# Optimization experiments

Measured on AMD Instinct MI355X. Metric: run time of the kernel, lower is better.

Reference implementation:

```python
import jax, jax.numpy as jnp
import numpy as np

EPS = 1e-5

def _layernorm(x, g, b):
    m = jnp.mean(x, axis=-1, keepdims=True)
    v = jnp.mean((x - m) ** 2, axis=-1, keepdims=True)
    return (x - m) * jax.lax.rsqrt(v + EPS) * g + b

def setup_inputs() -> dict:
    key = jax.random.key(0)
    ks = jax.random.split(key, 6)
    B, N, D, H, F = 4, 4096, 256, 256, 1024
    s = lambda d: 1.0 / np.sqrt(d)
    return {
        "x": jax.random.normal(ks[0], (B, N, D), jnp.float32),
        "ln1_g": jnp.ones((D,), jnp.float32),
        "ln1_b": jnp.zeros((D,), jnp.float32),
        "wq": jax.random.normal(ks[1], (D, H), jnp.float32) * s(D),
        "bq": jnp.zeros((H,), jnp.float32),
        "wk": jax.random.normal(ks[2], (D, H), jnp.float32) * s(D),
        "bk": jnp.zeros((H,), jnp.float32),
        "wv": jax.random.normal(ks[3], (D, D), jnp.float32) * s(D),
        "bv": jnp.zeros((D,), jnp.float32),
        "ln2_g": jnp.ones((D,), jnp.float32),
        "ln2_b": jnp.zeros((D,), jnp.float32),
        "w1": jax.random.normal(ks[4], (D, F), jnp.float32) * s(D),
        "b1": jnp.zeros((F,), jnp.float32),
        "w2": jax.random.normal(ks[5], (F, D), jnp.float32) * s(F),
        "b2": jnp.zeros((D,), jnp.float32),
    }

def reference(x, ln1_g, ln1_b, wq, bq, wk, bk, wv, bv, ln2_g, ln2_b, w1, b1, w2, b2):
    hdim = wq.shape[1]
    x = _layernorm(x, ln1_g, ln1_b)                      # [B,N,D]
    q = x @ wq + bq                                      # [B,N,H]
    k = x @ wk + bk                                      # [B,N,H]
    v = x @ wv + bv                                      # [B,N,D]
    att = jnp.einsum('bnh,bmh->bnm', q, k) / jnp.sqrt(jnp.float32(hdim))
    att = jax.nn.softmax(att, axis=-1)                   # [B,N,N]
    x = jnp.einsum('bnm,bmd->bnd', att, v) + x           # residual around attention
    h = _layernorm(x, ln2_g, ln2_b)
    h = jax.nn.relu(h @ w1 + b1) @ w2 + b2
    return h + x
```

## Files before the change

### kernel.cpp

```cpp
#include <hip/hip_runtime.h>
#include <stdint.h>

typedef unsigned short u16;
typedef __attribute__((ext_vector_type(8))) short short8;
typedef __attribute__((ext_vector_type(4))) float f32x4;
typedef __attribute__((ext_vector_type(16))) float f32x16;

__device__ __forceinline__ u16 f2b(float f){
  union { float f; unsigned u; } x; x.f = f;
  unsigned r = x.u + 0x7FFFu + ((x.u >> 16) & 1u);
  return (u16)(r >> 16);
}

__device__ __forceinline__ unsigned cvtpk_bf16(float lo, float hi){
  unsigned r;
  asm("v_cvt_pk_bf16_f32 %0, %1, %2" : "=v"(r) : "v"(lo), "v"(hi));
  return r;
}

__device__ __forceinline__ void gload_lds16(const void* g, void* l){
  __builtin_amdgcn_global_load_lds(
      (const __attribute__((address_space(1))) unsigned int*)g,
      (__attribute__((address_space(3))) unsigned int*)l, 16, 0, 0);
}

__global__ void __launch_bounds__(256) transpose_all(const float* __restrict__ wq,
                                                     const float* __restrict__ wk,
                                                     const float* __restrict__ wv,
                                                     const float* __restrict__ w1,
                                                     const float* __restrict__ w2,
                                                     u16* __restrict__ wqkvT,
                                                     u16* __restrict__ w1T,
                                                     u16* __restrict__ w2T){
  __shared__ float sm[32][33];
  int id = blockIdx.x;
  const float* in; u16* out; int K, N, kx, ny;
  if (id < 192){
    int j = id >> 6, r = id & 63;
    in = (j==0) ? wq : (j==1) ? wk : wv;
    out = wqkvT + (size_t)j*65536; K = 256; N = 256; kx = r>>3; ny = r&7;
  } else if (id < 448){
    int r = id - 192; in = w1; out = w1T; K = 256; N = 1024; kx = r&7; ny = r>>3;
  } else {
    int r = id - 448; in = w2; out = w2T; K = 1024; N = 256; kx = r>>3; ny = r&7;
  }
  int k0 = kx*32, n0 = ny*32;
  int t = threadIdx.x; int tr = t>>5, tc = t&31;
  #pragma unroll
  for (int p=0;p<4;p++) sm[p*8+tr][tc] = in[(size_t)(k0+p*8+tr)*N + n0+tc];
  __syncthreads();
  #pragma unroll
  for (int p=0;p<4;p++) out[(size_t)(n0+p*8+tr)*K + k0+tc] = f2b(sm[tc][p*8+tr]);
}

__global__ void __launch_bounds__(256) ln_kernel(const float* __restrict__ in,
                                                 const float* __restrict__ g,
                                                 const float* __restrict__ bb,
                                                 float* __restrict__ outF,
                                                 u16* __restrict__ outB){
  int row = blockIdx.x, t = threadIdx.x;
  size_t base = (size_t)row*256;
  float v = in[base + t];
  float s = v;
  #pragma unroll
  for (int m=1;m<64;m<<=1) s += __shfl_xor(s, m);
  __shared__ float red[4];
  int w = t>>6;
  if ((t&63)==0) red[w] = s;
  __syncthreads();
  float mean = (red[0]+red[1]+red[2]+red[3]) * (1.0f/256.0f);
  float d = v - mean;
  float s2 = d*d;
  #pragma unroll
  for (int m=1;m<64;m<<=1) s2 += __shfl_xor(s2, m);
  __syncthreads();
  if ((t&63)==0) red[w] = s2;
  __syncthreads();
  float var = (red[0]+red[1]+red[2]+red[3]) * (1.0f/256.0f);
  float y = d * rsqrtf(var + 1e-5f) * g[t] + bb[t];
  if (outF) outF[base+t] = y;
  outB[base+t] = f2b(y);
}

template<int MODE>
__global__ void __launch_bounds__(256, 2) gemm_bt(const u16* __restrict__ A,
                                                  const u16* __restrict__ BT,
                                                  const float* __restrict__ bias,
                                                  const float* __restrict__ bias2,
                                                  const float* __restrict__ bias3,
                                                  const float* __restrict__ res,
                                                  float* __restrict__ outF,
                                                  u16* __restrict__ outB,
                                                  u16* __restrict__ outB2,
                                                  u16* __restrict__ outB3,
                                                  int M, int N, int K){
  __shared__ u16 As[128*64];
  __shared__ u16 Bs[128*64];
  int tid = threadIdx.x;
  int m0 = blockIdx.x*128, n0 = blockIdx.y*128;
  int wave = tid>>6, lane = tid&63, lr = lane&15, lg = lane>>4;
  int wm = (wave>>1)*64, wn = (wave&1)*64;

  f32x4 acc[4][4];
  #pragma unroll
  for (int i=0;i<4;i++)
    #pragma unroll
    for (int j=0;j<4;j++) acc[i][j] = (f32x4){0.f,0.f,0.f,0.f};

  int nk = K >> 6;
  for (int kt=0; kt<nk; ++kt){
    __syncthreads();
    #pragma unroll
    for (int i=0;i<4;i++){
      int de = i*256 + tid; int row = de>>3; int ch = de&7; int sc = ch ^ (row&7);
      gload_lds16(A + (size_t)(m0+row)*K + kt*64 + sc*8, (char*)As + de*16);
    }
    #pragma unroll
    for (int i=0;i<4;i++){
      int de = i*256 + tid; int row = de>>3; int ch = de&7; int sc = ch ^ (row&7);
      gload_lds16(BT + (size_t)(n0+row)*K + kt*64 + sc*8, (char*)Bs + de*16);
    }
    asm volatile("s_waitcnt vmcnt(0)" ::: "memory");
    __syncthreads();
    #pragma unroll
    for (int kk=0;kk<2;kk++){
      short8 af[4], bf[4];
      #pragma unroll
      for (int mi=0;mi<4;mi++){
        int row = wm + mi*16 + lr;
        int c = (kk*4 + lg) ^ (row&7);
        af[mi] = *(const short8*)&As[row*64 + c*8];
      }
      #pragma unroll
      for (int ni=0;ni<4;ni++){
        int row = wn + ni*16 + lr;
        int c = (kk*4 + lg) ^ (row&7);
        bf[ni] = *(const short8*)&Bs[row*64 + c*8];
      }
      #pragma unroll
      for (int mi=0;mi<4;mi++)
        #pragma unroll
        for (int ni=0;ni<4;ni++)
          acc[mi][ni] = __builtin_amdgcn_mfma_f32_16x16x32_bf16(af[mi], bf[ni], acc[mi][ni], 0,0,0);
    }
  }
  #pragma unroll
  for (int mi=0;mi<4;mi++)
    #pragma unroll
    for (int ni=0;ni<4;ni++)
      #pragma unroll
      for (int r=0;r<4;r++){
        int row = m0 + wm + mi*16 + lg*4 + r;
        int col = n0 + wn + ni*16 + lr;
        if (MODE==3){
          int seg = n0 >> 8;
          int c2 = col & 255;
          float bb = (seg==0) ? bias[c2] : (seg==1) ? bias2[c2] : bias3[c2];
          float vout = acc[mi][ni][r] + bb;
          if (seg==0)      outB [(size_t)row*256 + c2] = f2b(vout);
          else if (seg==1) outB2[(size_t)row*256 + c2] = f2b(vout);
          else {
            size_t gaddr = ((size_t)(row>>12)<<20)
                         + ((((size_t)((row&4095)>>3)<<8) + (size_t)c2)<<3) + (row&7);
            outB3[gaddr] = f2b(vout);
          }
        } else {
          float vout = acc[mi][ni][r] + bias[col];
          if (MODE==1) vout = fmaxf(vout, 0.f);
          if (MODE==2) outF[(size_t)row*N + col] = vout + res[(size_t)row*N + col];
          else         outB[(size_t)row*N + col] = f2b(vout);
        }
      }
}

__device__ __forceinline__ void stage_tiles(const u16* __restrict__ Kb,
                                            const u16* __restrict__ Vt,
                                            int b, int kv0,
                                            char* Kdst, char* Vdst, int tid){
  #pragma unroll
  for (int i=0;i<4;i++){
    int de = i*256 + tid; int kv = de>>5; int c = de&31; int sc = c ^ (kv&7);
    gload_lds16(Kb + (((size_t)(b*4096 + kv0 + kv))<<8) + sc*8, Kdst + (size_t)de*16);
  }
  #pragma unroll
  for (int i=0;i<4;i++){
    int de = i*256 + tid; int kvc = de>>8; int d = de&255;
    gload_lds16(Vt + ((((size_t)b*512 + (kv0>>3) + kvc)<<8) + (size_t)d)*8,
                Vdst + (size_t)de*16);
  }
}

__global__ void __launch_bounds__(256, 2) flash_attn32(const u16* __restrict__ Qb,
                                                       const u16* __restrict__ Kb,
                                                       const u16* __restrict__ Vt,
                                                       u16* __restrict__ Opart,
                                                       float* __restrict__ MLpart){
  __shared__ __align__(16) char smem[74752];
  const int NC = 4096;
  int tid = threadIdx.x, wave = tid>>6, lane = tid&63;
  int lq = lane & 31, hi = lane >> 5;
  int b = blockIdx.y, s = blockIdx.z;
  int qb0 = blockIdx.x*128 + wave*32;
  int kvbeg = s*1024;
  const int NT = 32;
  u16* PsW = (u16*)(smem + 65536) + wave*32*36;

  short8 qf[16];
  {
    const u16* qbase = Qb + (((size_t)b*NC + qb0 + lq)<<8) + hi*8;
    #pragma unroll
    for (int ks=0; ks<16; ks++) qf[ks] = *(const short8*)(qbase + ks*16);
  }

  f32x16 o[8];
  #pragma unroll
  for (int i=0;i<8;i++)
    o[i] = (f32x16){0.f,0.f,0.f,0.f,0.f,0.f,0.f,0.f,0.f,0.f,0.f,0.f,0.f,0.f,0.f,0.f};
  float mrun = -__builtin_inff(), ell = 0.f;

  stage_tiles(Kb, Vt, b, kvbeg, smem, smem + 16384, tid);
  asm volatile("s_waitcnt vmcnt(0)" ::: "memory");
  __syncthreads();

  for (int t=0; t<NT; t++){
    char* Kc = smem + ((t&1) ? 32768 : 0);
    char* Vc = Kc + 16384;
    char* Kn = smem + ((t&1) ? 0 : 32768);
    char* Vn = Kn + 16384;
    int kv0 = kvbeg + t*32;
    if (t+1 < NT) stage_tiles(Kb, Vt, b, kv0+32, Kn, Vn, tid);

    f32x16 sacc = (f32x16){0.f,0.f,0.f,0.f,0.f,0.f,0.f,0.f,0.f,0.f,0.f,0.f,0.f,0.f,0.f,0.f};
    __builtin_amdgcn_s_setprio(1);
    #pragma unroll
    for (int ks=0; ks<16; ks++){
      int c = ks*2 + hi;
      short8 kf = *(const short8*)(Kc + lq*512 + ((c ^ (lq&7))<<4));
      sacc = __builtin_amdgcn_mfma_f32_32x32x16_bf16(kf, qf[ks], sacc, 0,0,0);
    }
    __builtin_amdgcn_s_setprio(0);

    float tmax = sacc[0];
    #pragma unroll
    for (int r=1;r<16;r++) tmax = fmaxf(tmax, sacc[r]);
    tmax *= 0.0625f;
    tmax = fmaxf(tmax, __shfl_xor(tmax, 32));
    if (!__all(tmax <= mrun + 8.f)){
      float mn = fmaxf(mrun, tmax);
      float sc = __expf(mrun - mn);
      mrun = mn; ell *= sc;
      #pragma unroll
      for (int r=0;r<16;r++){
        float scr = __shfl(sc, (r&3)+8*(r>>2)+4*hi);
        #pragma unroll
        for (int dt=0; dt<8; dt++) o[dt][r] *= scr;
      }
    }

    float rs = 0.f;
    #pragma unroll
    for (int h=0; h<2; h++){
      float p[8];
      #pragma unroll
      for (int r=0;r<8;r++){ p[r] = __expf(sacc[h*8+r]*0.0625f - mrun); rs += p[r]; }
      uint2 w0, w1;
      w0.x = cvtpk_bf16(p[0], p[1]);  w0.y = cvtpk_bf16(p[2], p[3]);
      w1.x = cvtpk_bf16(p[4], p[5]);  w1.y = cvtpk_bf16(p[6], p[7]);
      *(uint2*)(PsW + lq*36 + h*16 + hi*4)     = w0;
      *(uint2*)(PsW + lq*36 + h*16 + 8 + hi*4) = w1;
    }
    rs += __shfl_xor(rs, 32);
    ell += rs;
    asm volatile("s_waitcnt lgkmcnt(0)" ::: "memory");
    __builtin_amdgcn_sched_barrier(0);
    union { uint2 u2[2]; short8 s8; } pc0, pc1;
    pc0.u2[0] = *(const uint2*)(PsW + lq*36 + hi*8);
    pc0.u2[1] = *(const uint2*)(PsW + lq*36 + hi*8 + 4);
    pc1.u2[0] = *(const uint2*)(PsW + lq*36 + 16 + hi*8);
    pc1.u2[1] = *(const uint2*)(PsW + lq*36 + 16 + hi*8 + 4);
    short8 pa0 = pc0.s8, pa1 = pc1.s8;

    __builtin_amdgcn_s_setprio(1);
    #pragma unroll
    for (int dt=0; dt<8; dt++){
      short8 vf0 = *(const short8*)(Vc + (((hi  )*256 + dt*32 + lq)<<4));
      short8 vf1 = *(const short8*)(Vc + (((2+hi)*256 + dt*32 + lq)<<4));
      o[dt] = __builtin_amdgcn_mfma_f32_32x32x16_bf16(pa0, vf0, o[dt], 0,0,0);
      o[dt] = __builtin_amdgcn_mfma_f32_32x32x16_bf16(pa1, vf1, o[dt], 0,0,0);
    }
    __builtin_amdgcn_s_setprio(0);

    asm volatile("s_waitcnt vmcnt(0)" ::: "memory");
    __syncthreads();
  }

  size_t rowb = (size_t)s*16384 + (size_t)b*NC + qb0;
  #pragma unroll
  for (int dt=0; dt<8; dt++)
    #pragma unroll
    for (int r=0;r<16;r++){
      int q = (r&3) + 8*(r>>2) + 4*hi;
      Opart[(rowb + q)*256 + dt*32 + lq] = f2b(o[dt][r]);
    }
  if (lane < 32){
    MLpart[(rowb + lane)*2]     = mrun;
    MLpart[(rowb + lane)*2 + 1] = ell;
  }
}

__global__ void __launch_bounds__(256) merge4_ln(const u16* __restrict__ Opart,
                                                 const float* __restrict__ MLpart,
                                                 const float* __restrict__ xln,
                                                 const float* __restrict__ g2,
                                                 const float* __restrict__ be2,
                                                 float* __restrict__ x2,
                                                 u16* __restrict__ h2){
  int row = blockIdx.x; int t = threadIdx.x;
  const size_t RS = 16384ull*256;
  float m[4], l[4];
  #pragma unroll
  for (int s=0;s<4;s++){
    m[s] = MLpart[((size_t)s*16384 + row)*2];
    l[s] = MLpart[((size_t)s*16384 + row)*2 + 1];
  }
  float M = fmaxf(fmaxf(m[0],m[1]), fmaxf(m[2],m[3]));
  float e[4]; float den = 0.f;
  #pragma unroll
  for (int s=0;s<4;s++){ e[s] = __expf(m[s]-M); den += l[s]*e[s]; }
  float inv = 1.0f/den;
  size_t idx = (size_t)row*256 + t;
  float v = 0.f;
  #pragma unroll
  for (int s=0;s<4;s++){
    unsigned u = Opart[(size_t)s*RS + idx];
    v += __uint_as_float(u << 16) * e[s];
  }
  v = v*inv + xln[idx];
  x2[idx] = v;
  float s1 = v;
  #pragma unroll
  for (int mk=1;mk<64;mk<<=1) s1 += __shfl_xor(s1, mk);
  __shared__ float red[4];
  int w = t>>6;
  if ((t&63)==0) red[w] = s1;
  __syncthreads();
  float mean = (red[0]+red[1]+red[2]+red[3]) * (1.0f/256.0f);
  float d = v - mean;
  float s2 = d*d;
  #pragma unroll
  for (int mk=1;mk<64;mk<<=1) s2 += __shfl_xor(s2, mk);
  __syncthreads();
  if ((t&63)==0) red[w] = s2;
  __syncthreads();
  float var = (red[0]+red[1]+red[2]+red[3]) * (1.0f/256.0f);
  h2[idx] = f2b(d * rsqrtf(var + 1e-5f) * g2[t] + be2[t]);
}

extern "C" void kernel_launch(void* const* d_in, const int* in_sizes, int n_in,
                              void* d_out, int out_size, void* d_ws, size_t ws_size,
                              hipStream_t stream){
  const float* x   = (const float*)d_in[0];
  const float* g1  = (const float*)d_in[1];
  const float* be1 = (const float*)d_in[2];
  const float* wq  = (const float*)d_in[3];
  const float* bq  = (const float*)d_in[4];
  const float* wk  = (const float*)d_in[5];
  const float* bk  = (const float*)d_in[6];
  const float* wv  = (const float*)d_in[7];
  const float* bv  = (const float*)d_in[8];
  const float* g2  = (const float*)d_in[9];
  const float* be2 = (const float*)d_in[10];
  const float* w1  = (const float*)d_in[11];
  const float* bm1 = (const float*)d_in[12];
  const float* w2  = (const float*)d_in[13];
  const float* bm2 = (const float*)d_in[14];
  float* out = (float*)d_out;

  const size_t RS = 16384ull*256;
  char* p = (char*)d_ws;
  float* xln = (float*)p;  p += RS*4;
  u16*  Op   = (u16*)p;    p += 4*RS*2;
  float* ML  = (float*)p;  p += 4*16384ull*2*4;
  u16* xb  = (u16*)p; p += RS*2;
  u16* qb  = (u16*)p; p += RS*2;
  u16* kb  = (u16*)p; p += RS*2;
  u16* vT  = (u16*)p; p += RS*2;
  u16* wqkvT = (u16*)p; p += 3*65536ull*2;
  u16* w1T = (u16*)p; p += 262144ull*2;
  u16* w2T = (u16*)p; p += 262144ull*2;
  float* x2 = xln;
  u16*   h1 = Op;
  u16*   h2 = qb;

  transpose_all<<<704, 256, 0, stream>>>(wq, wk, wv, w1, w2, wqkvT, w1T, w2T);

  ln_kernel<<<16384,256,0,stream>>>(x, g1, be1, xln, xb);

  gemm_bt<3><<<dim3(128,6),256,0,stream>>>(xb, wqkvT, bq, bk, bv, nullptr, nullptr,
                                           qb, kb, vT, 16384,768,256);

  flash_attn32<<<dim3(32,4,4),256,0,stream>>>(qb, kb, vT, Op, ML);
  merge4_ln<<<16384,256,0,stream>>>(Op, ML, xln, g2, be2, x2, h2);

  gemm_bt<1><<<dim3(128,8),256,0,stream>>>(h2, w1T, bm1, nullptr, nullptr, nullptr, nullptr,
                                           h1, nullptr, nullptr, 16384,1024,256);
  gemm_bt<2><<<dim3(128,2),256,0,stream>>>(h1, w2T, bm2, nullptr, nullptr, x2, out,
                                           nullptr, nullptr, nullptr, 16384,256,1024);
}
```

Before: 168.7 us.

## Recompute LN1 in merge, store residual as bf16, use exp2 softmax

The fp32 LN1 output is no longer written to workspace. The merge kernel recomputes LN1 from x, and the post-attention residual x2 is stored as bf16 instead of fp32 for the final GEMM epilogue. This cuts HBM write and read traffic across several kernels. The softmax switches to exp2 with a folded log2e scale constant and a rescale threshold adjusted to match. Storing the residual in bf16 adds rounding error to the final output.

```diff
diff --git a/kernel.cpp b/kernel.cpp
--- a/kernel.cpp
+++ b/kernel.cpp
@@ -10,6 +10,9 @@
   union { float f; unsigned u; } x; x.f = f;
   unsigned r = x.u + 0x7FFFu + ((x.u >> 16) & 1u);
   return (u16)(r >> 16);
+}
+__device__ __forceinline__ float b2f(u16 u){
+  return __uint_as_float(((unsigned)u) << 16);
 }
 
 __device__ __forceinline__ unsigned cvtpk_bf16(float lo, float hi){
@@ -56,7 +59,6 @@
 __global__ void __launch_bounds__(256) ln_kernel(const float* __restrict__ in,
                                                  const float* __restrict__ g,
                                                  const float* __restrict__ bb,
-                                                 float* __restrict__ outF,
                                                  u16* __restrict__ outB){
   int row = blockIdx.x, t = threadIdx.x;
   size_t base = (size_t)row*256;
@@ -77,9 +79,7 @@
   if ((t&63)==0) red[w] = s2;
   __syncthreads();
   float var = (red[0]+red[1]+red[2]+red[3]) * (1.0f/256.0f);
-  float y = d * rsqrtf(var + 1e-5f) * g[t] + bb[t];
-  if (outF) outF[base+t] = y;
-  outB[base+t] = f2b(y);
+  outB[base+t] = f2b(d * rsqrtf(var + 1e-5f) * g[t] + bb[t]);
 }
 
 template<int MODE>
@@ -88,7 +88,7 @@
                                                   const float* __restrict__ bias,
                                                   const float* __restrict__ bias2,
                                                   const float* __restrict__ bias3,
-                                                  const float* __restrict__ res,
+                                                  const u16* __restrict__ res,
                                                   float* __restrict__ outF,
                                                   u16* __restrict__ outB,
                                                   u16* __restrict__ outB2,
@@ -167,7 +167,7 @@
         } else {
           float vout = acc[mi][ni][r] + bias[col];
           if (MODE==1) vout = fmaxf(vout, 0.f);
-          if (MODE==2) outF[(size_t)row*N + col] = vout + res[(size_t)row*N + col];
+          if (MODE==2) outF[(size_t)row*N + col] = vout + b2f(res[(size_t)row*N + col]);
           else         outB[(size_t)row*N + col] = f2b(vout);
         }
       }
@@ -197,6 +197,7 @@
                                                        float* __restrict__ MLpart){
   __shared__ __align__(16) char smem[74752];
   const int NC = 4096;
+  const float C2 = 0.09016844005555897f;
   int tid = threadIdx.x, wave = tid>>6, lane = tid&63;
   int lq = lane & 31, hi = lane >> 5;
   int b = blockIdx.y, s = blockIdx.z;
@@ -243,11 +244,11 @@
     float tmax = sacc[0];
     #pragma unroll
     for (int r=1;r<16;r++) tmax = fmaxf(tmax, sacc[r]);
-    tmax *= 0.0625f;
+    tmax *= C2;
     tmax = fmaxf(tmax, __shfl_xor(tmax, 32));
-    if (!__all(tmax <= mrun + 8.f)){
+    if (!__all(tmax <= mrun + 11.5f)){
       float mn = fmaxf(mrun, tmax);
-      float sc = __expf(mrun - mn);
+      float sc = exp2f(mrun - mn);
       mrun = mn; ell *= sc;
       #pragma unroll
       for (int r=0;r<16;r++){
@@ -262,7 +263,7 @@
     for (int h=0; h<2; h++){
       float p[8];
       #pragma unroll
-      for (int r=0;r<8;r++){ p[r] = __expf(sacc[h*8+r]*0.0625f - mrun); rs += p[r]; }
+      for (int r=0;r<8;r++){ p[r] = exp2f(fmaf(sacc[h*8+r], C2, -mrun)); rs += p[r]; }
       uint2 w0, w1;
       w0.x = cvtpk_bf16(p[0], p[1]);  w0.y = cvtpk_bf16(p[2], p[3]);
       w1.x = cvtpk_bf16(p[4], p[5]);  w1.y = cvtpk_bf16(p[6], p[7]);
@@ -310,13 +311,36 @@
 
 __global__ void __launch_bounds__(256) merge4_ln(const u16* __restrict__ Opart,
                                                  const float* __restrict__ MLpart,
-                                                 const float* __restrict__ xln,
+                                                 const float* __restrict__ x,
+                                                 const float* __restrict__ g1,
+                                                 const float* __restrict__ be1,
                                                  const float* __restrict__ g2,
                                                  const float* __restrict__ be2,
-                                                 float* __restrict__ x2,
+                                                 u16* __restrict__ x2b,
                                                  u16* __restrict__ h2){
   int row = blockIdx.x; int t = threadIdx.x;
   const size_t RS = 16384ull*256;
+  size_t idx = (size_t)row*256 + t;
+  __shared__ float red[4];
+  int w = t>>6;
+
+  float xv = x[idx];
+  float s1 = xv;
+  #pragma unroll
+  for (int mk=1;mk<64;mk<<=1) s1 += __shfl_xor(s1, mk);
+  if ((t&63)==0) red[w] = s1;
+  __syncthreads();
+  float mean1 = (red[0]+red[1]+red[2]+red[3]) * (1.0f/256.0f);
+  float d1 = xv - mean1;
+  float q1 = d1*d1;
+  #pragma unroll
+  for (int mk=1;mk<64;mk<<=1) q1 += __shfl_xor(q1, mk);
+  __syncthreads();
+  if ((t&63)==0) red[w] = q1;
+  __syncthreads();
+  float var1 = (red[0]+red[1]+red[2]+red[3]) * (1.0f/256.0f);
+  float xln = d1 * rsqrtf(var1 + 1e-5f) * g1[t] + be1[t];
+
   float m[4], l[4];
   #pragma unroll
   for (int s=0;s<4;s++){
@@ -326,34 +350,30 @@
   float M = fmaxf(fmaxf(m[0],m[1]), fmaxf(m[2],m[3]));
   float e[4]; float den = 0.f;
   #pragma unroll
-  for (int s=0;s<4;s++){ e[s] = __expf(m[s]-M); den += l[s]*e[s]; }
+  for (int s=0;s<4;s++){ e[s] = exp2f(m[s]-M); den += l[s]*e[s]; }
   float inv = 1.0f/den;
-  size_t idx = (size_t)row*256 + t;
   float v = 0.f;
   #pragma unroll
-  for (int s=0;s<4;s++){
-    unsigned u = Opart[(size_t)s*RS + idx];
-    v += __uint_as_float(u << 16) * e[s];
-  }
-  v = v*inv + xln[idx];
-  x2[idx] = v;
-  float s1 = v;
-  #pragma unroll
-  for (int mk=1;mk<64;mk<<=1) s1 += __shfl_xor(s1, mk);
-  __shared__ float red[4];
-  int w = t>>6;
-  if ((t&63)==0) red[w] = s1;
-  __syncthreads();
-  float mean = (red[0]+red[1]+red[2]+red[3]) * (1.0f/256.0f);
-  float d = v - mean;
-  float s2 = d*d;
+  for (int s=0;s<4;s++) v += b2f(Opart[(size_t)s*RS + idx]) * e[s];
+  v = v*inv + xln;
+  x2b[idx] = f2b(v);
+
+  float s2 = v;
   #pragma unroll
   for (int mk=1;mk<64;mk<<=1) s2 += __shfl_xor(s2, mk);
   __syncthreads();
   if ((t&63)==0) red[w] = s2;
   __syncthreads();
-  float var = (red[0]+red[1]+red[2]+red[3]) * (1.0f/256.0f);
-  h2[idx] = f2b(d * rsqrtf(var + 1e-5f) * g2[t] + be2[t]);
+  float mean2 = (red[0]+red[1]+red[2]+red[3]) * (1.0f/256.0f);
+  float d2 = v - mean2;
+  float q2 = d2*d2;
+  #pragma unroll
+  for (int mk=1;mk<64;mk<<=1) q2 += __shfl_xor(q2, mk);
+  __syncthreads();
+  if ((t&63)==0) red[w] = q2;
+  __syncthreads();
+  float var2 = (red[0]+red[1]+red[2]+red[3]) * (1.0f/256.0f);
+  h2[idx] = f2b(d2 * rsqrtf(var2 + 1e-5f) * g2[t] + be2[t]);
 }
 
 extern "C" void kernel_launch(void* const* d_in, const int* in_sizes, int n_in,
@@ -378,32 +398,31 @@
 
   const size_t RS = 16384ull*256;
   char* p = (char*)d_ws;
-  float* xln = (float*)p;  p += RS*4;
   u16*  Op   = (u16*)p;    p += 4*RS*2;
   float* ML  = (float*)p;  p += 4*16384ull*2*4;
   u16* xb  = (u16*)p; p += RS*2;
   u16* qb  = (u16*)p; p += RS*2;
   u16* kb  = (u16*)p; p += RS*2;
   u16* vT  = (u16*)p; p += RS*2;
+  u16* x2b = (u16*)p; p += RS*2;
   u16* wqkvT = (u16*)p; p += 3*65536ull*2;
   u16* w1T = (u16*)p; p += 262144ull*2;
   u16* w2T = (u16*)p; p += 262144ull*2;
-  float* x2 = xln;
   u16*   h1 = Op;
   u16*   h2 = qb;
 
   transpose_all<<<704, 256, 0, stream>>>(wq, wk, wv, w1, w2, wqkvT, w1T, w2T);
 
-  ln_kernel<<<16384,256,0,stream>>>(x, g1, be1, xln, xb);
+  ln_kernel<<<16384,256,0,stream>>>(x, g1, be1, xb);
 
   gemm_bt<3><<<dim3(128,6),256,0,stream>>>(xb, wqkvT, bq, bk, bv, nullptr, nullptr,
                                            qb, kb, vT, 16384,768,256);
 
   flash_attn32<<<dim3(32,4,4),256,0,stream>>>(qb, kb, vT, Op, ML);
-  merge4_ln<<<16384,256,0,stream>>>(Op, ML, xln, g2, be2, x2, h2);
+  merge4_ln<<<16384,256,0,stream>>>(Op, ML, x, g1, be1, g2, be2, x2b, h2);
 
   gemm_bt<1><<<dim3(128,8),256,0,stream>>>(h2, w1T, bm1, nullptr, nullptr, nullptr, nullptr,
                                            h1, nullptr, nullptr, 16384,1024,256);
-  gemm_bt<2><<<dim3(128,2),256,0,stream>>>(h1, w2T, bm2, nullptr, nullptr, x2, out,
+  gemm_bt<2><<<dim3(128,2),256,0,stream>>>(h1, w2T, bm2, nullptr, nullptr, x2b, out,
                                            nullptr, nullptr, nullptr, 16384,256,1024);
 }
```

Measured after the change: 182.0 us. 7.9% more time.
